# Kernel tuning notes

Hardware: AMD Instinct MI355X
Metric: run time of the kernel (lower is better)

Reference implementation:

```python
import jax, jax.numpy as jnp
import numpy as np

B = 4; D = 256; H = 8; L = 4; P = 4; DFF = 1024; DH = D // H
SHAPES = ((64, 64), (32, 32), (16, 16), (8, 8))
LEN = sum(h * w for h, w in SHAPES)  # 5440


def setup_inputs() -> dict:
    key = jax.random.key(0)
    ks = jax.random.split(key, 12)
    s = 0.02
    ss = jnp.array(SHAPES, jnp.int32)
    lsi = jnp.array(np.concatenate([[0], np.cumsum([h * w for h, w in SHAPES])[:-1]]), jnp.int32)
    return dict(
        src=jax.random.normal(ks[0], (B, LEN, D), jnp.float32),
        reference_points=jax.random.uniform(ks[1], (B, LEN, L, 2), jnp.float32),
        spatial_shapes=ss,
        level_start_index=lsi,
        padding_mask=jnp.zeros((B, LEN), bool),
        pos=jax.random.normal(ks[2], (B, LEN, D), jnp.float32),
        W_value=s * jax.random.normal(ks[3], (D, D), jnp.float32), b_value=jnp.zeros(D, jnp.float32),
        W_off=s * jax.random.normal(ks[4], (D, H * L * P * 2), jnp.float32), b_off=jnp.zeros(H * L * P * 2, jnp.float32),
        W_attn=s * jax.random.normal(ks[5], (D, H * L * P), jnp.float32), b_attn=jnp.zeros(H * L * P, jnp.float32),
        W_out=s * jax.random.normal(ks[6], (D, D), jnp.float32), b_out=jnp.zeros(D, jnp.float32),
        ln1_g=jnp.ones(D, jnp.float32), ln1_b=jnp.zeros(D, jnp.float32),
        W1=s * jax.random.normal(ks[7], (D, DFF), jnp.float32), b1=jnp.zeros(DFF, jnp.float32),
        W2=s * jax.random.normal(ks[8], (DFF, D), jnp.float32), b2=jnp.zeros(D, jnp.float32),
        ln2_g=jnp.ones(D, jnp.float32), ln2_b=jnp.zeros(D, jnp.float32),
    )


def layer_norm(x, g, b, eps=1e-5):
    m = jnp.mean(x, -1, keepdims=True)
    v = jnp.var(x, -1, keepdims=True)
    return (x - m) * jax.lax.rsqrt(v + eps) * g + b


def ms_deform_attn(query, src, reference_points, spatial_shapes, level_start_index, padding_mask,
                   W_value, b_value, W_off, b_off, W_attn, b_attn, W_out, b_out):
    Bq, Lq, C = query.shape
    Lin = src.shape[1]
    value = src @ W_value + b_value
    value = jnp.where(padding_mask[..., None], jnp.zeros((), value.dtype), value)
    value = value.reshape(Bq, Lin, H, DH).transpose(0, 2, 1, 3)  # [B,H,Lin,d]

    off = (query @ W_off + b_off).reshape(Bq, Lq, H, L, P, 2)
    attn = (query @ W_attn + b_attn).reshape(Bq, Lq, H, L * P)
    attn = jax.nn.softmax(attn, axis=-1).reshape(Bq, Lq, H, L, P)

    # offset normalizer is (W_l, H_l)
    norm = jnp.stack([spatial_shapes[:, 1], spatial_shapes[:, 0]], -1).astype(query.dtype)  # [L,2]
    loc = reference_points[:, :, None, :, None, :] + off / norm[None, None, None, :, None, :]  # [B,Lq,H,L,P,2]

    Hl = spatial_shapes[:, 0][None, None, None, :, None]  # [1,1,1,L,1]
    Wl = spatial_shapes[:, 1][None, None, None, :, None]
    start = level_start_index[None, None, None, :, None]
    # grid_sample align_corners=False: pixel = loc * size - 0.5
    px = loc[..., 0] * Wl.astype(query.dtype) - 0.5  # [B,Lq,H,L,P]
    py = loc[..., 1] * Hl.astype(query.dtype) - 0.5
    x0 = jnp.floor(px); y0 = jnp.floor(py)
    fx = px - x0; fy = py - y0
    x0i = x0.astype(jnp.int32); y0i = y0.astype(jnp.int32)

    out = jnp.zeros((Bq, Lq, H, DH), query.dtype)
    corners = ((0, 0, (1 - fx) * (1 - fy)), (1, 0, fx * (1 - fy)), (0, 1, (1 - fx) * fy), (1, 1, fx * fy))
    for dx, dy, cw in corners:
        xi = x0i + dx
        yi = y0i + dy
        valid = (xi >= 0) & (xi < Wl) & (yi >= 0) & (yi < Hl)  # zeros padding
        flat = start + jnp.clip(yi, 0, Hl - 1) * Wl + jnp.clip(xi, 0, Wl - 1)  # [B,Lq,H,L,P]
        w = attn * cw * valid.astype(query.dtype)  # [B,Lq,H,L,P]
        idx = flat.transpose(0, 2, 1, 3, 4).reshape(Bq, H, Lq * L * P)  # [B,H,N]
        g = jnp.take_along_axis(value, idx[..., None], axis=2)  # [B,H,N,d]
        g = g.reshape(Bq, H, Lq, L, P, DH)
        out = out + jnp.einsum('bqhlp,bhqlpd->bqhd', w, g)

    out = out.reshape(Bq, Lq, C)
    return out @ W_out + b_out


def reference(src, reference_points, spatial_shapes, level_start_index, padding_mask, pos,
              W_value, b_value, W_off, b_off, W_attn, b_attn, W_out, b_out,
              ln1_g, ln1_b, W1, b1, W2, b2, ln2_g, ln2_b):
    q = src + pos
    src2 = ms_deform_attn(q, src, reference_points, spatial_shapes, level_start_index, padding_mask,
                          W_value, b_value, W_off, b_off, W_attn, b_attn, W_out, b_out)
    x = layer_norm(src + src2, ln1_g, ln1_b)  # dropout is identity at eval
    ff = jax.nn.relu(x @ W1 + b1) @ W2 + b2
    return layer_norm(x + ff, ln2_g, ln2_b)
```

## Files before the change

kernel.cpp:

```cpp
#include <hip/hip_runtime.h>
#include <hip/hip_fp16.h>

constexpr int NB   = 4;
constexpr int SLEN = 5440;
constexpr long NTOK = (long)NB * SLEN;
constexpr int DD   = 256;
constexpr int NH   = 8;
constexpr int DHD  = 32;
constexpr int NL   = 4;
constexpr int NP   = 4;
constexpr int DFF  = 1024;

typedef __attribute__((ext_vector_type(8))) short short8;
typedef __attribute__((ext_vector_type(8))) unsigned short ushort8;
typedef __attribute__((ext_vector_type(4))) float f32x4;
typedef __attribute__((ext_vector_type(2))) float f32x2;

static __device__ __forceinline__ unsigned short f2bf(float x) {
  union { float f; unsigned int u; } v; v.f = x;
  unsigned int r = v.u + 0x7fffu + ((v.u >> 16) & 1u);
  return (unsigned short)(r >> 16);
}
static __device__ __forceinline__ float bf2f(unsigned short u) {
  union { unsigned int i; float f; } v; v.i = ((unsigned int)u) << 16; return v.f;
}
static __device__ __forceinline__ unsigned int pack2bf(float lo, float hi) {
  return (unsigned int)f2bf(lo) | ((unsigned int)f2bf(hi) << 16);
}
static __device__ __forceinline__ unsigned int pack2h(float a, float b) {
  return (unsigned int)__half_as_ushort(__float2half(a)) |
         ((unsigned int)__half_as_ushort(__float2half(b)) << 16);
}
static __device__ __forceinline__ float h2f(unsigned int u) {
  return __half2float(__ushort_as_half((unsigned short)(u & 0xffffu)));
}
static __device__ __forceinline__ f32x2 bf2x2(unsigned int u) {
  union { unsigned int i; float f; } a, b;
  a.i = u << 16; b.i = u & 0xffff0000u;
  f32x2 r; r[0] = a.f; r[1] = b.f; return r;
}

static __device__ __forceinline__ long fragpos(int k, int n, int KT) {
  const int kt = k >> 5, i = k & 7;
  const int lane = ((k >> 3) & 3) * 16 + (n & 15);
  const int nt = n >> 4;
  return (((long)(nt * KT + kt) * 64 + lane) * 8 + i);
}

__global__ __launch_bounds__(256) void k_prep_all(const float* __restrict__ W1,
                                                  const float* __restrict__ W2,
                                                  const float* __restrict__ Wv,
                                                  const float* __restrict__ Woff,
                                                  const float* __restrict__ Wattn,
                                                  const float* __restrict__ Wo,
                                                  unsigned short* __restrict__ W1f,
                                                  unsigned short* __restrict__ W2f,
                                                  unsigned short* __restrict__ Wvf,
                                                  unsigned short* __restrict__ Wqf,
                                                  unsigned short* __restrict__ Wof) {
  const int g = blockIdx.x * 256 + threadIdx.x;
  if (g < 262144) {
    const int k = g >> 10, n = g & 1023;
    W1f[fragpos(k, n, 8)] = f2bf(W1[g]);
  } else if (g < 524288) {
    const int g2 = g - 262144;
    const int k = g2 >> 8, n = g2 & 255;
    W2f[fragpos(k, n, 32)] = f2bf(W2[g2]);
  } else if (g < 589824) {
    const int g2 = g - 524288;
    const int k = g2 >> 8, n = g2 & 255;
    Wvf[fragpos(k, n, 8)] = f2bf(Wv[g2]);
  } else if (g < 688128) {
    const int g2 = g - 589824;
    const int k = g2 / 384, n = g2 % 384;
    const float w = (n < 256) ? Woff[k * 256 + n] : Wattn[k * 128 + (n - 256)];
    Wqf[fragpos(k, n, 8)] = f2bf(w);
  } else if (g < 753664) {
    const int g2 = g - 688128;
    const int k = g2 >> 8, n = g2 & 255;
    Wof[fragpos(k, n, 8)] = f2bf(Wo[g2]);
  }
}

__global__ __launch_bounds__(256) void k_value_mfma(const float* __restrict__ src,
                                                    const unsigned short* __restrict__ Wvf,
                                                    const float* __restrict__ bv,
                                                    unsigned short* __restrict__ valbf) {
  __shared__ unsigned short Xs[32 * 256];
  const int t = threadIdx.x;
  const int w = t >> 6, lane = t & 63;
  const int lr = lane & 15, lgrp = lane >> 4;
  const long row0 = (long)blockIdx.x * 32;
  {
    const int r = t >> 3;
    const int c0 = (t & 7) * 32;
    const float* srcp = &src[(row0 + r) * DD + c0];
#pragma unroll
    for (int j = 0; j < 4; ++j) {
      const float4 a = *reinterpret_cast<const float4*>(&srcp[j * 8 + 0]);
      const float4 b = *reinterpret_cast<const float4*>(&srcp[j * 8 + 4]);
      short8 pk;
      pk[0] = (short)f2bf(a.x); pk[1] = (short)f2bf(a.y);
      pk[2] = (short)f2bf(a.z); pk[3] = (short)f2bf(a.w);
      pk[4] = (short)f2bf(b.x); pk[5] = (short)f2bf(b.y);
      pk[6] = (short)f2bf(b.z); pk[7] = (short)f2bf(b.w);
      int byte = r * 512 + (c0 + j * 8) * 2;
      byte ^= (r & 7) << 4;
      *reinterpret_cast<short8*>(reinterpret_cast<char*>(Xs) + byte) = pk;
    }
  }
  __syncthreads();
  short8 af[2][8];
#pragma unroll
  for (int mt = 0; mt < 2; ++mt)
#pragma unroll
    for (int kt = 0; kt < 8; ++kt) {
      const int row = mt * 16 + lr;
      int byte = row * 512 + kt * 64 + lgrp * 16;
      byte ^= (row & 7) << 4;
      af[mt][kt] = *reinterpret_cast<const short8*>(reinterpret_cast<const char*>(Xs) + byte);
    }
  f32x4 acc[2][4];
#pragma unroll
  for (int mt = 0; mt < 2; ++mt)
#pragma unroll
    for (int n = 0; n < 4; ++n) acc[mt][n] = (f32x4){0.f, 0.f, 0.f, 0.f};
#pragma unroll
  for (int n = 0; n < 4; ++n) {
    const int nt = w * 4 + n;
#pragma unroll
    for (int kt = 0; kt < 8; ++kt) {
      const short8 bf_ = *reinterpret_cast<const short8*>(&Wvf[((nt * 8 + kt) * 64 + lane) * 8]);
#pragma unroll
      for (int mt = 0; mt < 2; ++mt)
        acc[mt][n] = __builtin_amdgcn_mfma_f32_16x16x32_bf16(af[mt][kt], bf_, acc[mt][n], 0, 0, 0);
    }
  }
#pragma unroll
  for (int n = 0; n < 4; ++n) {
    const int col = w * 64 + n * 16 + lr;
    const float bb = bv[col];
#pragma unroll
    for (int mt = 0; mt < 2; ++mt)
#pragma unroll
      for (int j = 0; j < 4; ++j) {
        const int row = mt * 16 + lgrp * 4 + j;
        valbf[(row0 + row) * DD + col] = f2bf(acc[mt][n][j] + bb);
      }
  }
}

__global__ __launch_bounds__(256) void k_qproj_mfma(const float* __restrict__ src,
                                                    const float* __restrict__ pos,
                                                    const unsigned short* __restrict__ Wqf,
                                                    const float* __restrict__ boff,
                                                    const float* __restrict__ battn,
                                                    unsigned short* __restrict__ offbf,
                                                    float* __restrict__ attn) {
  __shared__ unsigned short Xs[32 * 256];
  const int t = threadIdx.x;
  const int w = t >> 6, lane = t & 63;
  const int lr = lane & 15, lgrp = lane >> 4;
  const long row0 = (long)blockIdx.x * 32;
  {
    const int r = t >> 3;
    const int c0 = (t & 7) * 32;
    const float* sp = &src[(row0 + r) * DD + c0];
    const float* pp = &pos[(row0 + r) * DD + c0];
#pragma unroll
    for (int j = 0; j < 4; ++j) {
      const float4 a = *reinterpret_cast<const float4*>(&sp[j * 8 + 0]);
      const float4 b = *reinterpret_cast<const float4*>(&sp[j * 8 + 4]);
      const float4 c = *reinterpret_cast<const float4*>(&pp[j * 8 + 0]);
      const float4 d = *reinterpret_cast<const float4*>(&pp[j * 8 + 4]);
      short8 pk;
      pk[0] = (short)f2bf(a.x + c.x); pk[1] = (short)f2bf(a.y + c.y);
      pk[2] = (short)f2bf(a.z + c.z); pk[3] = (short)f2bf(a.w + c.w);
      pk[4] = (short)f2bf(b.x + d.x); pk[5] = (short)f2bf(b.y + d.y);
      pk[6] = (short)f2bf(b.z + d.z); pk[7] = (short)f2bf(b.w + d.w);
      int byte = r * 512 + (c0 + j * 8) * 2;
      byte ^= (r & 7) << 4;
      *reinterpret_cast<short8*>(reinterpret_cast<char*>(Xs) + byte) = pk;
    }
  }
  __syncthreads();
  short8 af[2][8];
#pragma unroll
  for (int mt = 0; mt < 2; ++mt)
#pragma unroll
    for (int kt = 0; kt < 8; ++kt) {
      const int row = mt * 16 + lr;
      int byte = row * 512 + kt * 64 + lgrp * 16;
      byte ^= (row & 7) << 4;
      af[mt][kt] = *reinterpret_cast<const short8*>(reinterpret_cast<const char*>(Xs) + byte);
    }
  f32x4 acc[2][6];
#pragma unroll
  for (int mt = 0; mt < 2; ++mt)
#pragma unroll
    for (int i = 0; i < 6; ++i) acc[mt][i] = (f32x4){0.f, 0.f, 0.f, 0.f};
#pragma unroll
  for (int i = 0; i < 6; ++i) {
    const int ntg = w * 6 + i;
#pragma unroll
    for (int kt = 0; kt < 8; ++kt) {
      const short8 bf_ = *reinterpret_cast<const short8*>(&Wqf[((ntg * 8 + kt) * 64 + lane) * 8]);
#pragma unroll
      for (int mt = 0; mt < 2; ++mt)
        acc[mt][i] = __builtin_amdgcn_mfma_f32_16x16x32_bf16(af[mt][kt], bf_, acc[mt][i], 0, 0, 0);
    }
  }
#pragma unroll
  for (int i = 0; i < 6; ++i) {
    const int ntg = w * 6 + i;
    if (ntg < 16) {
      const int col = ntg * 16 + lr;
      const float bb = boff[col];
#pragma unroll
      for (int mt = 0; mt < 2; ++mt)
#pragma unroll
        for (int j = 0; j < 4; ++j) {
          const int row = mt * 16 + lgrp * 4 + j;
          offbf[(row0 + row) * 256 + col] = f2bf(acc[mt][i][j] + bb);
        }
    } else {
      const int na = ntg - 16;
      const float bb = battn[na * 16 + lr];
#pragma unroll
      for (int mt = 0; mt < 2; ++mt)
#pragma unroll
        for (int j = 0; j < 4; ++j) {
          const int row = mt * 16 + lgrp * 4 + j;
          const float v = acc[mt][i][j] + bb;
          float m = v;
#pragma unroll
          for (int d_ = 1; d_ <= 8; d_ <<= 1) m = fmaxf(m, __shfl_xor(m, d_, 16));
          const float e = __expf(v - m);
          float s = e;
#pragma unroll
          for (int d_ = 1; d_ <= 8; d_ <<= 1) s += __shfl_xor(s, d_, 16);
          attn[(row0 + row) * 128 + na * 16 + lr] = e / s;
        }
    }
  }
}

__global__ __launch_bounds__(256) void k_sample5(const unsigned short* __restrict__ valbf,
                                                 const unsigned short* __restrict__ offbf,
                                                 const float* __restrict__ attn,
                                                 const float* __restrict__ refp,
                                                 unsigned short* __restrict__ src2bf) {
  __shared__ int4  sIdx[4][2][8][16];
  __shared__ uint2 sWgt[4][2][8][16];
  const int t = threadIdx.x;
  const int w = t >> 6, lane = t & 63;
  const int tok = lane >> 5, hg = (lane >> 2) & 7, li = lane & 3;
  const int B = blockIdx.x;
  const int bimg = (B & 7) >> 1;
  const int ii = ((B >> 3) << 1) + (B & 1);
  const long n = (long)bimg * SLEN + ii * 8 + w * 2 + tok;
  const long bOff = (long)bimg * SLEN;

  const int   WlA[4] = {64, 32, 16, 8};
  const float rWA[4] = {1.f / 64.f, 1.f / 32.f, 1.f / 16.f, 1.f / 8.f};
  const int   stA[4] = {0, 4096, 5120, 5376};

#pragma unroll
  for (int q = 0; q < 4; ++q) {
    const int pt = q * 4 + li;
    const int Wi = WlA[q];
    const float Wf = (float)Wi, rW = rWA[q];
    const float rx = refp[(n * 4 + q) * 2 + 0];
    const float ry = refp[(n * 4 + q) * 2 + 1];
    const float aw = attn[n * 128 + hg * 16 + pt];
    const int oi = ((hg * 4 + q) * 4 + li) * 2;
    const unsigned int opk = *reinterpret_cast<const unsigned int*>(&offbf[n * 256 + oi]);
    const float ox = bf2f((unsigned short)(opk & 0xffff));
    const float oy = bf2f((unsigned short)(opk >> 16));
    const float px = (rx + ox * rW) * Wf - 0.5f;
    const float py = (ry + oy * rW) * Wf - 0.5f;
    const float x0f = floorf(px), y0f = floorf(py);
    const float fx = px - x0f, fy = py - y0f;
    const int x0 = (int)x0f, y0 = (int)y0f;
    int   ic[4];
    float wc[4];
#pragma unroll
    for (int c = 0; c < 4; ++c) {
      const int dx = c & 1, dy = c >> 1;
      const int xi = x0 + dx, yi = y0 + dy;
      const float cw = (dx ? fx : 1.f - fx) * (dy ? fy : 1.f - fy);
      const bool valid = (xi >= 0) && (xi < Wi) && (yi >= 0) && (yi < Wi);
      const int xc = min(max(xi, 0), Wi - 1);
      const int yc = min(max(yi, 0), Wi - 1);
      const long flat = stA[q] + yc * Wi + xc;
      ic[c] = (int)((bOff + flat) * DD + hg * DHD);
      wc[c] = aw * cw * (valid ? 1.f : 0.f);
    }
    const int slot = pt ^ hg;
    sIdx[w][tok][hg][slot] = make_int4(ic[0], ic[1], ic[2], ic[3]);
    sWgt[w][tok][hg][slot] = make_uint2(pack2h(wc[0], wc[1]), pack2h(wc[2], wc[3]));
  }
  __syncthreads();

  f32x2 acc2[4];
#pragma unroll
  for (int d = 0; d < 4; ++d) acc2[d] = (f32x2){0.f, 0.f};
#pragma unroll 4
  for (int pt = 0; pt < 16; ++pt) {
    const int slot = pt ^ hg;
    const int4  ia = sIdx[w][tok][hg][slot];
    const uint2 wp = sWgt[w][tok][hg][slot];
    const float w0 = h2f(wp.x), w1 = h2f(wp.x >> 16);
    const float w2 = h2f(wp.y), w3 = h2f(wp.y >> 16);
    const uint4 u0 = *reinterpret_cast<const uint4*>(&valbf[(long)ia.x + li * 8]);
    const uint4 u1 = *reinterpret_cast<const uint4*>(&valbf[(long)ia.y + li * 8]);
    const uint4 u2 = *reinterpret_cast<const uint4*>(&valbf[(long)ia.z + li * 8]);
    const uint4 u3 = *reinterpret_cast<const uint4*>(&valbf[(long)ia.w + li * 8]);
    const f32x2 wv0 = {w0, w0}, wv1 = {w1, w1}, wv2 = {w2, w2}, wv3 = {w3, w3};
    acc2[0] += wv0 * bf2x2(u0.x) + wv1 * bf2x2(u1.x) + wv2 * bf2x2(u2.x) + wv3 * bf2x2(u3.x);
    acc2[1] += wv0 * bf2x2(u0.y) + wv1 * bf2x2(u1.y) + wv2 * bf2x2(u2.y) + wv3 * bf2x2(u3.y);
    acc2[2] += wv0 * bf2x2(u0.z) + wv1 * bf2x2(u1.z) + wv2 * bf2x2(u2.z) + wv3 * bf2x2(u3.z);
    acc2[3] += wv0 * bf2x2(u0.w) + wv1 * bf2x2(u1.w) + wv2 * bf2x2(u2.w) + wv3 * bf2x2(u3.w);
  }
  ushort8 o;
#pragma unroll
  for (int d = 0; d < 4; ++d) {
    o[2 * d]     = f2bf(acc2[d][0]);
    o[2 * d + 1] = f2bf(acc2[d][1]);
  }
  *reinterpret_cast<ushort8*>(&src2bf[n * DD + hg * DHD + li * 8]) = o;
}

__global__ __launch_bounds__(256) void k_outproj_mfma(const unsigned short* __restrict__ src2bf,
                                                      const unsigned short* __restrict__ Wof,
                                                      const float* __restrict__ bo,
                                                      const float* __restrict__ src,
                                                      const float* __restrict__ g1,
                                                      const float* __restrict__ b1g,
                                                      unsigned short* __restrict__ xbf) {
  __shared__ float rsum[32][4];
  __shared__ float rssq[32][4];
  const int t = threadIdx.x;
  const int w = t >> 6, lane = t & 63;
  const int lr = lane & 15, lgrp = lane >> 4;
  const long row0 = (long)blockIdx.x * 32;

  short8 af[2][8];
#pragma unroll
  for (int mt = 0; mt < 2; ++mt)
#pragma unroll
    for (int kt = 0; kt < 8; ++kt)
      af[mt][kt] = *reinterpret_cast<const short8*>(
          &src2bf[(row0 + mt * 16 + lr) * DD + kt * 32 + lgrp * 8]);

  f32x4 acc[2][4];
#pragma unroll
  for (int mt = 0; mt < 2; ++mt)
#pragma unroll
    for (int n = 0; n < 4; ++n) acc[mt][n] = (f32x4){0.f, 0.f, 0.f, 0.f};
#pragma unroll
  for (int n = 0; n < 4; ++n) {
    const int nt = w * 4 + n;
#pragma unroll
    for (int kt = 0; kt < 8; ++kt) {
      const short8 bf_ = *reinterpret_cast<const short8*>(&Wof[((nt * 8 + kt) * 64 + lane) * 8]);
#pragma unroll
      for (int mt = 0; mt < 2; ++mt)
        acc[mt][n] = __builtin_amdgcn_mfma_f32_16x16x32_bf16(af[mt][kt], bf_, acc[mt][n], 0, 0, 0);
    }
  }
  float bc[4], gc[4], bgc[4];
#pragma unroll
  for (int n = 0; n < 4; ++n) {
    const int col = w * 64 + n * 16 + lr;
    bc[n] = bo[col]; gc[n] = g1[col]; bgc[n] = b1g[col];
  }
  float vals[2][4][4];
#pragma unroll
  for (int mt = 0; mt < 2; ++mt)
#pragma unroll
    for (int j = 0; j < 4; ++j) {
      const int row = mt * 16 + lgrp * 4 + j;
      float s = 0.f, ss = 0.f;
#pragma unroll
      for (int n = 0; n < 4; ++n) {
        const int col = w * 64 + n * 16 + lr;
        const float v = acc[mt][n][j] + bc[n] + src[(row0 + row) * DD + col];
        vals[mt][n][j] = v;
        s += v; ss += v * v;
      }
#pragma unroll
      for (int m = 1; m <= 8; m <<= 1) { s += __shfl_xor(s, m, 64); ss += __shfl_xor(ss, m, 64); }
      if (lr == 0) { rsum[row][w] = s; rssq[row][w] = ss; }
    }
  __syncthreads();
#pragma unroll
  for (int mt = 0; mt < 2; ++mt)
#pragma unroll
    for (int j = 0; j < 4; ++j) {
      const int row = mt * 16 + lgrp * 4 + j;
      const float s  = rsum[row][0] + rsum[row][1] + rsum[row][2] + rsum[row][3];
      const float ss = rssq[row][0] + rssq[row][1] + rssq[row][2] + rssq[row][3];
      const float mean = s * (1.f / 256.f);
      const float inv  = rsqrtf(ss * (1.f / 256.f) - mean * mean + 1e-5f);
#pragma unroll
      for (int n = 0; n < 4; ++n) {
        const int col = w * 64 + n * 16 + lr;
        xbf[(row0 + row) * DD + col] = f2bf((vals[mt][n][j] - mean) * inv * gc[n] + bgc[n]);
      }
    }
}

__global__ __launch_bounds__(256) void k_ffn1e(const unsigned short* __restrict__ xbf,
                                               const unsigned short* __restrict__ W1f,
                                               const float* __restrict__ b1v,
                                               unsigned short* __restrict__ hfrag) {
  const int t = threadIdx.x;
  const int w = t >> 6, lane = t & 63;
  const int lr = lane & 15, lgrp = lane >> 4;
  const long row0 = (long)blockIdx.x * 64;
  const int hg = blockIdx.y;

  f32x4 acc[8][4];
#pragma unroll
  for (int mm = 0; mm < 8; ++mm)
#pragma unroll
    for (int n = 0; n < 4; ++n) acc[mm][n] = (f32x4){0.f, 0.f, 0.f, 0.f};

#pragma unroll
  for (int kt = 0; kt < 8; ++kt) {
    short8 bx[4];
#pragma unroll
    for (int n = 0; n < 4; ++n)
      bx[n] = *reinterpret_cast<const short8*>(
          &xbf[(row0 + n * 16 + lr) * DD + kt * 32 + lgrp * 8]);
#pragma unroll
    for (int mm = 0; mm < 8; ++mm) {
      const int ntg = hg * 32 + w * 8 + mm;
      const short8 aw1 = *reinterpret_cast<const short8*>(&W1f[((ntg * 8 + kt) * 64 + lane) * 8]);
#pragma unroll
      for (int n = 0; n < 4; ++n)
        acc[mm][n] = __builtin_amdgcn_mfma_f32_16x16x32_bf16(aw1, bx[n], acc[mm][n], 0, 0, 0);
    }
  }

#pragma unroll
  for (int mm = 0; mm < 8; ++mm) {
    const int ht = hg * 32 + w * 8 + mm;
    const float4 bq = *reinterpret_cast<const float4*>(&b1v[ht * 16 + lgrp * 4]);
#pragma unroll
    for (int n = 0; n < 4; ++n) {
      const long tt = (long)blockIdx.x * 4 + n;
      const long tbase = (tt * 64 + ht) * 256;
      int2 pk;
      pk.x = (int)pack2bf(fmaxf(acc[mm][n][0] + bq.x, 0.f),
                          fmaxf(acc[mm][n][1] + bq.y, 0.f));
      pk.y = (int)pack2bf(fmaxf(acc[mm][n][2] + bq.z, 0.f),
                          fmaxf(acc[mm][n][3] + bq.w, 0.f));
      *reinterpret_cast<int2*>(&hfrag[tbase + lane * 4]) = pk;
    }
  }
}

__global__ __launch_bounds__(256) void k_ffn2t(const unsigned short* __restrict__ hfrag,
                                               const unsigned short* __restrict__ W2f,
                                               const float* __restrict__ b2v_,
                                               const unsigned short* __restrict__ xbf,
                                               const float* __restrict__ g2,
                                               const float* __restrict__ b2g,
                                               float* __restrict__ outp) {
  __shared__ float rsum[32][4];
  __shared__ float rssq[32][4];
  const int t = threadIdx.x;
  const int w = t >> 6, lane = t & 63;
  const int lr = lane & 15, lgrp = lane >> 4;
  const long row0 = (long)blockIdx.x * 32;

  f32x4 acc[2][4];
#pragma unroll
  for (int mt = 0; mt < 2; ++mt)
#pragma unroll
    for (int n = 0; n < 4; ++n) acc[mt][n] = (f32x4){0.f, 0.f, 0.f, 0.f};

#pragma unroll 4
  for (int kt = 0; kt < 32; ++kt) {
    short8 ha[2];
#pragma unroll
    for (int mt = 0; mt < 2; ++mt) {
      const long tt = (row0 >> 4) + mt;
      const long tb = (tt * 64 + kt * 2 + (lgrp >> 1)) * 256;
      const unsigned short* tp = &hfrag[tb + (lgrp & 1) * 128 + lr * 4];
      union { short8 s8; struct { int2 lo, hi; } p; } u;
      u.p.lo = *reinterpret_cast<const int2*>(tp);
      u.p.hi = *reinterpret_cast<const int2*>(tp + 64);
      ha[mt] = u.s8;
    }
#pragma unroll
    for (int n = 0; n < 4; ++n) {
      const int nt = w * 4 + n;
      const short8 bf_ = *reinterpret_cast<const short8*>(&W2f[((nt * 32 + kt) * 64 + lane) * 8]);
#pragma unroll
      for (int mt = 0; mt < 2; ++mt)
        acc[mt][n] = __builtin_amdgcn_mfma_f32_16x16x32_bf16(ha[mt], bf_, acc[mt][n], 0, 0, 0);
    }
  }

  float b2c[4], g2c[4], bgc[4];
#pragma unroll
  for (int n = 0; n < 4; ++n) {
    const int col = w * 64 + n * 16 + lr;
    b2c[n] = b2v_[col]; g2c[n] = g2[col]; bgc[n] = b2g[col];
  }
  float vals[2][4][4];
#pragma unroll
  for (int mt = 0; mt < 2; ++mt)
#pragma unroll
    for (int j = 0; j < 4; ++j) {
      const int row = mt * 16 + lgrp * 4 + j;
      float s = 0.f, ss = 0.f;
#pragma unroll
      for (int n = 0; n < 4; ++n) {
        const int col = w * 64 + n * 16 + lr;
        const float v = acc[mt][n][j] + b2c[n] + bf2f(xbf[(row0 + row) * DD + col]);
        vals[mt][n][j] = v;
        s += v; ss += v * v;
      }
#pragma unroll
      for (int m = 1; m <= 8; m <<= 1) { s += __shfl_xor(s, m, 64); ss += __shfl_xor(ss, m, 64); }
      if (lr == 0) { rsum[row][w] = s; rssq[row][w] = ss; }
    }
  __syncthreads();
#pragma unroll
  for (int mt = 0; mt < 2; ++mt)
#pragma unroll
    for (int j = 0; j < 4; ++j) {
      const int row = mt * 16 + lgrp * 4 + j;
      const float s  = rsum[row][0] + rsum[row][1] + rsum[row][2] + rsum[row][3];
      const float ss = rssq[row][0] + rssq[row][1] + rssq[row][2] + rssq[row][3];
      const float mean = s * (1.f / 256.f);
      const float inv  = rsqrtf(ss * (1.f / 256.f) - mean * mean + 1e-5f);
#pragma unroll
      for (int n = 0; n < 4; ++n) {
        const int col = w * 64 + n * 16 + lr;
        outp[(row0 + row) * DD + col] = (vals[mt][n][j] - mean) * inv * g2c[n] + bgc[n];
      }
    }
}

extern "C" void kernel_launch(void* const* d_in, const int* in_sizes, int n_in,
                              void* d_out, int out_size, void* d_ws, size_t ws_size,
                              hipStream_t stream) {
  const float* src  = (const float*)d_in[0];
  const float* refp = (const float*)d_in[1];
  const float* pos  = (const float*)d_in[5];
  const float* Wv   = (const float*)d_in[6];
  const float* bv   = (const float*)d_in[7];
  const float* Woff = (const float*)d_in[8];
  const float* boff = (const float*)d_in[9];
  const float* Wat  = (const float*)d_in[10];
  const float* bat  = (const float*)d_in[11];
  const float* Wo   = (const float*)d_in[12];
  const float* bo   = (const float*)d_in[13];
  const float* g1   = (const float*)d_in[14];
  const float* b1g  = (const float*)d_in[15];
  const float* W1   = (const float*)d_in[16];
  const float* b1f  = (const float*)d_in[17];
  const float* W2   = (const float*)d_in[18];
  const float* b2f  = (const float*)d_in[19];
  const float* g2   = (const float*)d_in[20];
  const float* b2g  = (const float*)d_in[21];
  float* out = (float*)d_out;

  unsigned short* valbf  = (unsigned short*)d_ws;
  unsigned short* offbf  = valbf + NTOK * 256;
  float*          attn   = (float*)(offbf + NTOK * 256);
  unsigned short* src2bf = (unsigned short*)(attn + NTOK * 128);
  unsigned short* xbf    = src2bf + NTOK * 256;
  unsigned short* W1f = xbf + NTOK * 256;
  unsigned short* W2f = W1f + 262144;
  unsigned short* Wvf = W2f + 262144;
  unsigned short* Wqf = Wvf + 65536;
  unsigned short* Wof = Wqf + 98304;
  unsigned short* frag_end = Wof + 65536;
  const size_t used  = (size_t)((char*)frag_end - (char*)d_ws);
  const size_t hneed = (size_t)NTOK * 1024 * 2;
  unsigned short* hfrag = (used + hneed <= ws_size) ? frag_end
                                                    : (unsigned short*)d_ws;

  hipLaunchKernelGGL(k_prep_all, dim3(2944), dim3(256), 0, stream,
                     W1, W2, Wv, Woff, Wat, Wo, W1f, W2f, Wvf, Wqf, Wof);
  hipLaunchKernelGGL(k_value_mfma, dim3((int)(NTOK / 32)), dim3(256), 0, stream,
                     src, Wvf, bv, valbf);
  hipLaunchKernelGGL(k_qproj_mfma, dim3((int)(NTOK / 32)), dim3(256), 0, stream,
                     src, pos, Wqf, boff, bat, offbf, attn);
  hipLaunchKernelGGL(k_sample5, dim3((int)(NTOK / 8)), dim3(256), 0, stream,
                     valbf, offbf, attn, refp, src2bf);
  hipLaunchKernelGGL(k_outproj_mfma, dim3((int)(NTOK / 32)), dim3(256), 0, stream,
                     src2bf, Wof, bo, src, g1, b1g, xbf);
  hipLaunchKernelGGL(k_ffn1e, dim3((int)(NTOK / 64), 2), dim3(256), 0, stream,
                     xbf, W1f, b1f, hfrag);
  hipLaunchKernelGGL(k_ffn2t, dim3((int)(NTOK / 32)), dim3(256), 0, stream,
                     hfrag, W2f, b2f, xbf, g2, b2g, out);
}
```

Before: 182.0 us.

## Fuse value and query projections; store value as fp16 and sample with packed half FMA

Merges the value projection and the offset/attention projection into one kernel, so each block reads src once, stages both src and src+pos tiles in shared memory, and runs both MFMA GEMMs. The value tensor is now written as fp16 instead of bf16, and the sampling kernel accumulates with packed __hfma2 using duplicated half weights rather than converting to fp32 pairs. This removes one launch and a duplicate src read, and cuts ALU conversion work in the gather loop. In exchange it doubles shared memory per block, which may lower occupancy, and accumulating in fp16 costs precision.

```diff
diff --git a/kernel.cpp b/kernel.cpp
--- a/kernel.cpp
+++ b/kernel.cpp
@@ -14,7 +14,6 @@
 typedef __attribute__((ext_vector_type(8))) short short8;
 typedef __attribute__((ext_vector_type(8))) unsigned short ushort8;
 typedef __attribute__((ext_vector_type(4))) float f32x4;
-typedef __attribute__((ext_vector_type(2))) float f32x2;
 
 static __device__ __forceinline__ unsigned short f2bf(float x) {
   union { float f; unsigned int u; } v; v.f = x;
@@ -27,17 +26,12 @@
 static __device__ __forceinline__ unsigned int pack2bf(float lo, float hi) {
   return (unsigned int)f2bf(lo) | ((unsigned int)f2bf(hi) << 16);
 }
-static __device__ __forceinline__ unsigned int pack2h(float a, float b) {
-  return (unsigned int)__half_as_ushort(__float2half(a)) |
-         ((unsigned int)__half_as_ushort(__float2half(b)) << 16);
-}
-static __device__ __forceinline__ float h2f(unsigned int u) {
-  return __half2float(__ushort_as_half((unsigned short)(u & 0xffffu)));
-}
-static __device__ __forceinline__ f32x2 bf2x2(unsigned int u) {
-  union { unsigned int i; float f; } a, b;
-  a.i = u << 16; b.i = u & 0xffff0000u;
-  f32x2 r; r[0] = a.f; r[1] = b.f; return r;
+static __device__ __forceinline__ unsigned int pack2h_dup(float a) {
+  const unsigned int h = (unsigned int)__half_as_ushort(__float2half(a));
+  return h | (h << 16);
+}
+static __device__ __forceinline__ __half2 u2h2(unsigned int u) {
+  union { unsigned int i; __half2 h; } c; c.i = u; return c.h;
 }
 
 static __device__ __forceinline__ long fragpos(int k, int n, int KT) {
@@ -82,82 +76,18 @@
   }
 }
 
-__global__ __launch_bounds__(256) void k_value_mfma(const float* __restrict__ src,
-                                                    const unsigned short* __restrict__ Wvf,
-                                                    const float* __restrict__ bv,
-                                                    unsigned short* __restrict__ valbf) {
+__global__ __launch_bounds__(256) void k_vq(const float* __restrict__ src,
+                                            const float* __restrict__ pos,
+                                            const unsigned short* __restrict__ Wvf,
+                                            const float* __restrict__ bv,
+                                            const unsigned short* __restrict__ Wqf,
+                                            const float* __restrict__ boff,
+                                            const float* __restrict__ battn,
+                                            unsigned short* __restrict__ valh,
+                                            unsigned short* __restrict__ offbf,
+                                            float* __restrict__ attn) {
   __shared__ unsigned short Xs[32 * 256];
-  const int t = threadIdx.x;
-  const int w = t >> 6, lane = t & 63;
-  const int lr = lane & 15, lgrp = lane >> 4;
-  const long row0 = (long)blockIdx.x * 32;
-  {
-    const int r = t >> 3;
-    const int c0 = (t & 7) * 32;
-    const float* srcp = &src[(row0 + r) * DD + c0];
-#pragma unroll
-    for (int j = 0; j < 4; ++j) {
-      const float4 a = *reinterpret_cast<const float4*>(&srcp[j * 8 + 0]);
-      const float4 b = *reinterpret_cast<const float4*>(&srcp[j * 8 + 4]);
-      short8 pk;
-      pk[0] = (short)f2bf(a.x); pk[1] = (short)f2bf(a.y);
-      pk[2] = (short)f2bf(a.z); pk[3] = (short)f2bf(a.w);
-      pk[4] = (short)f2bf(b.x); pk[5] = (short)f2bf(b.y);
-      pk[6] = (short)f2bf(b.z); pk[7] = (short)f2bf(b.w);
-      int byte = r * 512 + (c0 + j * 8) * 2;
-      byte ^= (r & 7) << 4;
-      *reinterpret_cast<short8*>(reinterpret_cast<char*>(Xs) + byte) = pk;
-    }
-  }
-  __syncthreads();
-  short8 af[2][8];
-#pragma unroll
-  for (int mt = 0; mt < 2; ++mt)
-#pragma unroll
-    for (int kt = 0; kt < 8; ++kt) {
-      const int row = mt * 16 + lr;
-      int byte = row * 512 + kt * 64 + lgrp * 16;
-      byte ^= (row & 7) << 4;
-      af[mt][kt] = *reinterpret_cast<const short8*>(reinterpret_cast<const char*>(Xs) + byte);
-    }
-  f32x4 acc[2][4];
-#pragma unroll
-  for (int mt = 0; mt < 2; ++mt)
-#pragma unroll
-    for (int n = 0; n < 4; ++n) acc[mt][n] = (f32x4){0.f, 0.f, 0.f, 0.f};
-#pragma unroll
-  for (int n = 0; n < 4; ++n) {
-    const int nt = w * 4 + n;
-#pragma unroll
-    for (int kt = 0; kt < 8; ++kt) {
-      const short8 bf_ = *reinterpret_cast<const short8*>(&Wvf[((nt * 8 + kt) * 64 + lane) * 8]);
-#pragma unroll
-      for (int mt = 0; mt < 2; ++mt)
-        acc[mt][n] = __builtin_amdgcn_mfma_f32_16x16x32_bf16(af[mt][kt], bf_, acc[mt][n], 0, 0, 0);
-    }
-  }
-#pragma unroll
-  for (int n = 0; n < 4; ++n) {
-    const int col = w * 64 + n * 16 + lr;
-    const float bb = bv[col];
-#pragma unroll
-    for (int mt = 0; mt < 2; ++mt)
-#pragma unroll
-      for (int j = 0; j < 4; ++j) {
-        const int row = mt * 16 + lgrp * 4 + j;
-        valbf[(row0 + row) * DD + col] = f2bf(acc[mt][n][j] + bb);
-      }
-  }
-}
-
-__global__ __launch_bounds__(256) void k_qproj_mfma(const float* __restrict__ src,
-                                                    const float* __restrict__ pos,
-                                                    const unsigned short* __restrict__ Wqf,
-                                                    const float* __restrict__ boff,
-                                                    const float* __restrict__ battn,
-                                                    unsigned short* __restrict__ offbf,
-                                                    float* __restrict__ attn) {
-  __shared__ unsigned short Xs[32 * 256];
+  __shared__ unsigned short Qs[32 * 256];
   const int t = threadIdx.x;
   const int w = t >> 6, lane = t & 63;
   const int lr = lane & 15, lgrp = lane >> 4;
@@ -173,85 +103,135 @@
       const float4 b = *reinterpret_cast<const float4*>(&sp[j * 8 + 4]);
       const float4 c = *reinterpret_cast<const float4*>(&pp[j * 8 + 0]);
       const float4 d = *reinterpret_cast<const float4*>(&pp[j * 8 + 4]);
-      short8 pk;
-      pk[0] = (short)f2bf(a.x + c.x); pk[1] = (short)f2bf(a.y + c.y);
-      pk[2] = (short)f2bf(a.z + c.z); pk[3] = (short)f2bf(a.w + c.w);
-      pk[4] = (short)f2bf(b.x + d.x); pk[5] = (short)f2bf(b.y + d.y);
-      pk[6] = (short)f2bf(b.z + d.z); pk[7] = (short)f2bf(b.w + d.w);
+      short8 pkx, pkq;
+      pkx[0] = (short)f2bf(a.x); pkx[1] = (short)f2bf(a.y);
+      pkx[2] = (short)f2bf(a.z); pkx[3] = (short)f2bf(a.w);
+      pkx[4] = (short)f2bf(b.x); pkx[5] = (short)f2bf(b.y);
+      pkx[6] = (short)f2bf(b.z); pkx[7] = (short)f2bf(b.w);
+      pkq[0] = (short)f2bf(a.x + c.x); pkq[1] = (short)f2bf(a.y + c.y);
+      pkq[2] = (short)f2bf(a.z + c.z); pkq[3] = (short)f2bf(a.w + c.w);
+      pkq[4] = (short)f2bf(b.x + d.x); pkq[5] = (short)f2bf(b.y + d.y);
+      pkq[6] = (short)f2bf(b.z + d.z); pkq[7] = (short)f2bf(b.w + d.w);
       int byte = r * 512 + (c0 + j * 8) * 2;
       byte ^= (r & 7) << 4;
-      *reinterpret_cast<short8*>(reinterpret_cast<char*>(Xs) + byte) = pk;
+      *reinterpret_cast<short8*>(reinterpret_cast<char*>(Xs) + byte) = pkx;
+      *reinterpret_cast<short8*>(reinterpret_cast<char*>(Qs) + byte) = pkq;
     }
   }
   __syncthreads();
-  short8 af[2][8];
-#pragma unroll
-  for (int mt = 0; mt < 2; ++mt)
-#pragma unroll
-    for (int kt = 0; kt < 8; ++kt) {
-      const int row = mt * 16 + lr;
-      int byte = row * 512 + kt * 64 + lgrp * 16;
-      byte ^= (row & 7) << 4;
-      af[mt][kt] = *reinterpret_cast<const short8*>(reinterpret_cast<const char*>(Xs) + byte);
-    }
-  f32x4 acc[2][6];
-#pragma unroll
-  for (int mt = 0; mt < 2; ++mt)
-#pragma unroll
-    for (int i = 0; i < 6; ++i) acc[mt][i] = (f32x4){0.f, 0.f, 0.f, 0.f};
-#pragma unroll
-  for (int i = 0; i < 6; ++i) {
-    const int ntg = w * 6 + i;
-#pragma unroll
-    for (int kt = 0; kt < 8; ++kt) {
-      const short8 bf_ = *reinterpret_cast<const short8*>(&Wqf[((ntg * 8 + kt) * 64 + lane) * 8]);
-#pragma unroll
-      for (int mt = 0; mt < 2; ++mt)
-        acc[mt][i] = __builtin_amdgcn_mfma_f32_16x16x32_bf16(af[mt][kt], bf_, acc[mt][i], 0, 0, 0);
-    }
-  }
-#pragma unroll
-  for (int i = 0; i < 6; ++i) {
-    const int ntg = w * 6 + i;
-    if (ntg < 16) {
-      const int col = ntg * 16 + lr;
-      const float bb = boff[col];
+
+  {
+    short8 af[2][8];
+#pragma unroll
+    for (int mt = 0; mt < 2; ++mt)
+#pragma unroll
+      for (int kt = 0; kt < 8; ++kt) {
+        const int row = mt * 16 + lr;
+        int byte = row * 512 + kt * 64 + lgrp * 16;
+        byte ^= (row & 7) << 4;
+        af[mt][kt] = *reinterpret_cast<const short8*>(reinterpret_cast<const char*>(Xs) + byte);
+      }
+    f32x4 acc[2][4];
+#pragma unroll
+    for (int mt = 0; mt < 2; ++mt)
+#pragma unroll
+      for (int n = 0; n < 4; ++n) acc[mt][n] = (f32x4){0.f, 0.f, 0.f, 0.f};
+#pragma unroll
+    for (int n = 0; n < 4; ++n) {
+      const int nt = w * 4 + n;
+#pragma unroll
+      for (int kt = 0; kt < 8; ++kt) {
+        const short8 bf_ = *reinterpret_cast<const short8*>(&Wvf[((nt * 8 + kt) * 64 + lane) * 8]);
+#pragma unroll
+        for (int mt = 0; mt < 2; ++mt)
+          acc[mt][n] = __builtin_amdgcn_mfma_f32_16x16x32_bf16(af[mt][kt], bf_, acc[mt][n], 0, 0, 0);
+      }
+    }
+#pragma unroll
+    for (int n = 0; n < 4; ++n) {
+      const int col = w * 64 + n * 16 + lr;
+      const float bb = bv[col];
 #pragma unroll
       for (int mt = 0; mt < 2; ++mt)
 #pragma unroll
         for (int j = 0; j < 4; ++j) {
           const int row = mt * 16 + lgrp * 4 + j;
-          offbf[(row0 + row) * 256 + col] = f2bf(acc[mt][i][j] + bb);
+          valh[(row0 + row) * DD + col] =
+              __half_as_ushort(__float2half(acc[mt][n][j] + bb));
         }
-    } else {
-      const int na = ntg - 16;
-      const float bb = battn[na * 16 + lr];
-#pragma unroll
-      for (int mt = 0; mt < 2; ++mt)
-#pragma unroll
-        for (int j = 0; j < 4; ++j) {
-          const int row = mt * 16 + lgrp * 4 + j;
-          const float v = acc[mt][i][j] + bb;
-          float m = v;
-#pragma unroll
-          for (int d_ = 1; d_ <= 8; d_ <<= 1) m = fmaxf(m, __shfl_xor(m, d_, 16));
-          const float e = __expf(v - m);
-          float s = e;
-#pragma unroll
-          for (int d_ = 1; d_ <= 8; d_ <<= 1) s += __shfl_xor(s, d_, 16);
-          attn[(row0 + row) * 128 + na * 16 + lr] = e / s;
-        }
-    }
-  }
-}
-
-__global__ __launch_bounds__(256) void k_sample5(const unsigned short* __restrict__ valbf,
+    }
+  }
+
+  {
+    short8 af[2][8];
+#pragma unroll
+    for (int mt = 0; mt < 2; ++mt)
+#pragma unroll
+      for (int kt = 0; kt < 8; ++kt) {
+        const int row = mt * 16 + lr;
+        int byte = row * 512 + kt * 64 + lgrp * 16;
+        byte ^= (row & 7) << 4;
+        af[mt][kt] = *reinterpret_cast<const short8*>(reinterpret_cast<const char*>(Qs) + byte);
+      }
+    f32x4 acc[2][6];
+#pragma unroll
+    for (int mt = 0; mt < 2; ++mt)
+#pragma unroll
+      for (int i = 0; i < 6; ++i) acc[mt][i] = (f32x4){0.f, 0.f, 0.f, 0.f};
+#pragma unroll
+    for (int i = 0; i < 6; ++i) {
+      const int ntg = w * 6 + i;
+#pragma unroll
+      for (int kt = 0; kt < 8; ++kt) {
+        const short8 bf_ = *reinterpret_cast<const short8*>(&Wqf[((ntg * 8 + kt) * 64 + lane) * 8]);
+#pragma unroll
+        for (int mt = 0; mt < 2; ++mt)
+          acc[mt][i] = __builtin_amdgcn_mfma_f32_16x16x32_bf16(af[mt][kt], bf_, acc[mt][i], 0, 0, 0);
+      }
+    }
+#pragma unroll
+    for (int i = 0; i < 6; ++i) {
+      const int ntg = w * 6 + i;
+      if (ntg < 16) {
+        const int col = ntg * 16 + lr;
+        const float bb = boff[col];
+#pragma unroll
+        for (int mt = 0; mt < 2; ++mt)
+#pragma unroll
+          for (int j = 0; j < 4; ++j) {
+            const int row = mt * 16 + lgrp * 4 + j;
+            offbf[(row0 + row) * 256 + col] = f2bf(acc[mt][i][j] + bb);
+          }
+      } else {
+        const int na = ntg - 16;
+        const float bb = battn[na * 16 + lr];
+#pragma unroll
+        for (int mt = 0; mt < 2; ++mt)
+#pragma unroll
+          for (int j = 0; j < 4; ++j) {
+            const int row = mt * 16 + lgrp * 4 + j;
+            const float v = acc[mt][i][j] + bb;
+            float m = v;
+#pragma unroll
+            for (int d_ = 1; d_ <= 8; d_ <<= 1) m = fmaxf(m, __shfl_xor(m, d_, 16));
+            const float e = __expf(v - m);
+            float s = e;
+#pragma unroll
+            for (int d_ = 1; d_ <= 8; d_ <<= 1) s += __shfl_xor(s, d_, 16);
+            attn[(row0 + row) * 128 + na * 16 + lr] = e / s;
+          }
+      }
+    }
+  }
+}
+
+__global__ __launch_bounds__(256) void k_sample6(const unsigned short* __restrict__ valh,
                                                  const unsigned short* __restrict__ offbf,
                                                  const float* __restrict__ attn,
                                                  const float* __restrict__ refp,
                                                  unsigned short* __restrict__ src2bf) {
   __shared__ int4  sIdx[4][2][8][16];
-  __shared__ uint2 sWgt[4][2][8][16];
+  __shared__ uint4 sWgt[4][2][8][16];
   const int t = threadIdx.x;
   const int w = t >> 6, lane = t & 63;
   const int tok = lane >> 5, hg = (lane >> 2) & 7, li = lane & 3;
@@ -298,35 +278,46 @@
     }
     const int slot = pt ^ hg;
     sIdx[w][tok][hg][slot] = make_int4(ic[0], ic[1], ic[2], ic[3]);
-    sWgt[w][tok][hg][slot] = make_uint2(pack2h(wc[0], wc[1]), pack2h(wc[2], wc[3]));
+    sWgt[w][tok][hg][slot] = make_uint4(pack2h_dup(wc[0]), pack2h_dup(wc[1]),
+                                        pack2h_dup(wc[2]), pack2h_dup(wc[3]));
   }
   __syncthreads();
 
-  f32x2 acc2[4];
-#pragma unroll
-  for (int d = 0; d < 4; ++d) acc2[d] = (f32x2){0.f, 0.f};
+  __half2 acc[4];
+#pragma unroll
+  for (int d = 0; d < 4; ++d) acc[d] = __float2half2_rn(0.f);
 #pragma unroll 4
   for (int pt = 0; pt < 16; ++pt) {
     const int slot = pt ^ hg;
     const int4  ia = sIdx[w][tok][hg][slot];
-    const uint2 wp = sWgt[w][tok][hg][slot];
-    const float w0 = h2f(wp.x), w1 = h2f(wp.x >> 16);
-    const float w2 = h2f(wp.y), w3 = h2f(wp.y >> 16);
-    const uint4 u0 = *reinterpret_cast<const uint4*>(&valbf[(long)ia.x + li * 8]);
-    const uint4 u1 = *reinterpret_cast<const uint4*>(&valbf[(long)ia.y + li * 8]);
-    const uint4 u2 = *reinterpret_cast<const uint4*>(&valbf[(long)ia.z + li * 8]);
-    const uint4 u3 = *reinterpret_cast<const uint4*>(&valbf[(long)ia.w + li * 8]);
-    const f32x2 wv0 = {w0, w0}, wv1 = {w1, w1}, wv2 = {w2, w2}, wv3 = {w3, w3};
-    acc2[0] += wv0 * bf2x2(u0.x) + wv1 * bf2x2(u1.x) + wv2 * bf2x2(u2.x) + wv3 * bf2x2(u3.x);
-    acc2[1] += wv0 * bf2x2(u0.y) + wv1 * bf2x2(u1.y) + wv2 * bf2x2(u2.y) + wv3 * bf2x2(u3.y);
-    acc2[2] += wv0 * bf2x2(u0.z) + wv1 * bf2x2(u1.z) + wv2 * bf2x2(u2.z) + wv3 * bf2x2(u3.z);
-    acc2[3] += wv0 * bf2x2(u0.w) + wv1 * bf2x2(u1.w) + wv2 * bf2x2(u2.w) + wv3 * bf2x2(u3.w);
+    const uint4 wp = sWgt[w][tok][hg][slot];
+    const uint4 u0 = *reinterpret_cast<const uint4*>(&valh[(long)ia.x + li * 8]);
+    const uint4 u1 = *reinterpret_cast<const uint4*>(&valh[(long)ia.y + li * 8]);
+    const uint4 u2 = *reinterpret_cast<const uint4*>(&valh[(long)ia.z + li * 8]);
+    const uint4 u3 = *reinterpret_cast<const uint4*>(&valh[(long)ia.w + li * 8]);
+    const __half2 w0 = u2h2(wp.x), w1 = u2h2(wp.y), w2 = u2h2(wp.z), w3 = u2h2(wp.w);
+    acc[0] = __hfma2(u2h2(u0.x), w0, acc[0]);
+    acc[1] = __hfma2(u2h2(u0.y), w0, acc[1]);
+    acc[2] = __hfma2(u2h2(u0.z), w0, acc[2]);
+    acc[3] = __hfma2(u2h2(u0.w), w0, acc[3]);
+    acc[0] = __hfma2(u2h2(u1.x), w1, acc[0]);
+    acc[1] = __hfma2(u2h2(u1.y), w1, acc[1]);
+    acc[2] = __hfma2(u2h2(u1.z), w1, acc[2]);
+    acc[3] = __hfma2(u2h2(u1.w), w1, acc[3]);
+    acc[0] = __hfma2(u2h2(u2.x), w2, acc[0]);
+    acc[1] = __hfma2(u2h2(u2.y), w2, acc[1]);
+    acc[2] = __hfma2(u2h2(u2.z), w2, acc[2]);
+    acc[3] = __hfma2(u2h2(u2.w), w2, acc[3]);
+    acc[0] = __hfma2(u2h2(u3.x), w3, acc[0]);
+    acc[1] = __hfma2(u2h2(u3.y), w3, acc[1]);
+    acc[2] = __hfma2(u2h2(u3.z), w3, acc[2]);
+    acc[3] = __hfma2(u2h2(u3.w), w3, acc[3]);
   }
   ushort8 o;
 #pragma unroll
   for (int d = 0; d < 4; ++d) {
-    o[2 * d]     = f2bf(acc2[d][0]);
-    o[2 * d + 1] = f2bf(acc2[d][1]);
+    o[2 * d]     = f2bf(__half2float(__low2half(acc[d])));
+    o[2 * d + 1] = f2bf(__half2float(__high2half(acc[d])));
   }
   *reinterpret_cast<ushort8*>(&src2bf[n * DD + hg * DHD + li * 8]) = o;
 }
@@ -571,8 +562,8 @@
   const float* b2g  = (const float*)d_in[21];
   float* out = (float*)d_out;
 
-  unsigned short* valbf  = (unsigned short*)d_ws;
-  unsigned short* offbf  = valbf + NTOK * 256;
+  unsigned short* valh   = (unsigned short*)d_ws;
+  unsigned short* offbf  = valh + NTOK * 256;
   float*          attn   = (float*)(offbf + NTOK * 256);
   unsigned short* src2bf = (unsigned short*)(attn + NTOK * 128);
   unsigned short* xbf    = src2bf + NTOK * 256;
@@ -589,12 +580,10 @@
 
   hipLaunchKernelGGL(k_prep_all, dim3(2944), dim3(256), 0, stream,
                      W1, W2, Wv, Woff, Wat, Wo, W1f, W2f, Wvf, Wqf, Wof);
-  hipLaunchKernelGGL(k_value_mfma, dim3((int)(NTOK / 32)), dim3(256), 0, stream,
-                     src, Wvf, bv, valbf);
-  hipLaunchKernelGGL(k_qproj_mfma, dim3((int)(NTOK / 32)), dim3(256), 0, stream,
-                     src, pos, Wqf, boff, bat, offbf, attn);
-  hipLaunchKernelGGL(k_sample5, dim3((int)(NTOK / 8)), dim3(256), 0, stream,
-                     valbf, offbf, attn, refp, src2bf);
+  hipLaunchKernelGGL(k_vq, dim3((int)(NTOK / 32)), dim3(256), 0, stream,
+                     src, pos, Wvf, bv, Wqf, boff, bat, valh, offbf, attn);
+  hipLaunchKernelGGL(k_sample6, dim3((int)(NTOK / 8)), dim3(256), 0, stream,
+                     valh, offbf, attn, refp, src2bf);
   hipLaunchKernelGGL(k_outproj_mfma, dim3((int)(NTOK / 32)), dim3(256), 0, stream,
                      src2bf, Wof, bo, src, g1, b1g, xbf);
   hipLaunchKernelGGL(k_ffn1e, dim3((int)(NTOK / 64), 2), dim3(256), 0, stream,
```

Result: faster. 171.8 us (-5.6%).
